# Optimization experiments

Hardware: AMD Instinct MI355X
Metric: run time of the kernel (lower is better)

Reference implementation:

```python
import jax, jax.numpy as jnp
import numpy as np

HIDDEN = 512
HEADS = 8
HEAD_DIM = HIDDEN // HEADS


def setup_inputs() -> dict:
    key = jax.random.key(0)
    ks = jax.random.split(key, 12)
    B, S = 2, 2048
    s = 1.0 / np.sqrt(HIDDEN)
    inp = {
        "query": jax.random.normal(ks[0], (B, S, HIDDEN), dtype=jnp.float32),
        "key": jax.random.normal(ks[1], (B, S, HIDDEN), dtype=jnp.float32),
        "value": jax.random.normal(ks[2], (B, S, HIDDEN), dtype=jnp.float32),
        "Wq": jax.random.uniform(ks[3], (HIDDEN, HIDDEN), jnp.float32, -s, s),
        "bq": jnp.zeros((HIDDEN,), jnp.float32),
        "Wk": jax.random.uniform(ks[4], (HIDDEN, HIDDEN), jnp.float32, -s, s),
        "bk": jnp.zeros((HIDDEN,), jnp.float32),
        "Wv": jax.random.uniform(ks[5], (HIDDEN, HIDDEN), jnp.float32, -s, s),
        "bv": jnp.zeros((HIDDEN,), jnp.float32),
        "Wo": jax.random.uniform(ks[6], (HIDDEN, HIDDEN), jnp.float32, -s, s),
        "bo": jnp.zeros((HIDDEN,), jnp.float32),
    }
    return inp


def reference(query, key, value, Wq, bq, Wk, bk, Wv, bv, Wo, bo):
    B, S, _ = query.shape
    scale = jnp.sqrt(jnp.asarray(HEAD_DIM, dtype=query.dtype))
    # Linear projections (torch Linear: x @ W.T + b)
    Q = (query @ Wq.T + bq).reshape(B, S, HEADS, HEAD_DIM).transpose(0, 2, 1, 3)
    K = (key @ Wk.T + bk).reshape(B, S, HEADS, HEAD_DIM).transpose(0, 2, 1, 3)
    V = (value @ Wv.T + bv).reshape(B, S, HEADS, HEAD_DIM).transpose(0, 2, 1, 3)
    # Scores: [B, H, S, S]
    energy = jnp.einsum("bhqd,bhkd->bhqk", Q, K) / scale
    attn = jax.nn.softmax(energy, axis=-1)
    # Dropout is identity in eval mode.
    x = jnp.einsum("bhqk,bhkd->bhqd", attn, V)
    x = x.transpose(0, 2, 1, 3).reshape(B, S, HIDDEN)
    return x @ Wo.T + bo
```

## Files before the change

kernel.cpp:

```cpp
#include <hip/hip_runtime.h>

typedef __bf16 bf16x8 __attribute__((ext_vector_type(8)));
typedef float f32x4 __attribute__((ext_vector_type(4)));
typedef unsigned int uint4v __attribute__((ext_vector_type(4)));
typedef unsigned int uint2v __attribute__((ext_vector_type(2)));

__device__ __forceinline__ unsigned short f2bf(float f) {
  union { float f; unsigned int u; } v; v.f = f;
  unsigned int u = v.u;
  u += 0x7FFFu + ((u >> 16) & 1u);
  return (unsigned short)(u >> 16);
}

__device__ __forceinline__ unsigned int pack2bf(float a, float b) {
  return (unsigned int)f2bf(a) | ((unsigned int)f2bf(b) << 16);
}

__device__ __forceinline__ unsigned int packtrunc(float a, float b) {
  return __builtin_amdgcn_perm(__float_as_uint(b), __float_as_uint(a),
                               0x07060302u);
}

__global__ __launch_bounds__(256) void convert_w(
    const float* wq, const float* wk, const float* wv, const float* wo,
    unsigned short* wqc, unsigned short* wkc, unsigned short* wvc,
    unsigned short* woc, float qscale)
{
  const float* src; unsigned short* dst; float sc = 1.f;
  switch (blockIdx.y) {
    case 0: src = wq; dst = wqc; sc = qscale; break;
    case 1: src = wk; dst = wkc; break;
    case 2: src = wv; dst = wvc; break;
    default: src = wo; dst = woc; break;
  }
  int idx = (blockIdx.x * 256 + threadIdx.x) * 8;
  f32x4 a = *(const f32x4*)(src + idx);
  f32x4 b = *(const f32x4*)(src + idx + 4);
  uint4v p;
  p.x = pack2bf(a.x * sc, a.y * sc);
  p.y = pack2bf(a.z * sc, a.w * sc);
  p.z = pack2bf(b.x * sc, b.y * sc);
  p.w = pack2bf(b.z * sc, b.w * sc);
  *(uint4v*)(dst + idx) = p;
}

template<int OUT, bool AF32>
__device__ __forceinline__ void gemm_core(
    const void* __restrict__ Ap, const unsigned short* __restrict__ W,
    const float* __restrict__ bias, void* __restrict__ Cp,
    float bscale, int mbase, int nbase)
{
  __shared__ union {
    struct { unsigned short As[2][64][40]; unsigned short Bs[2][128][40]; } t;
    unsigned short Cs[128][72];
  } u;

  const int tid  = threadIdx.x;
  const int wave = tid >> 6, lane = tid & 63;
  const int lrow = lane & 15, lgrp = lane >> 4;
  const int ar = tid >> 2, ac = (tid & 3) * 8;

  const unsigned short* Bg0 = W + (size_t)(nbase + ar) * 512 + ac;
  const unsigned short* Bg1 = W + (size_t)(nbase + ar + 64) * 512 + ac;

  f32x4 acc[4][2];
#pragma unroll
  for (int i = 0; i < 4; i++)
#pragma unroll
    for (int j = 0; j < 2; j++) acc[i][j] = (f32x4){0.f, 0.f, 0.f, 0.f};

  const unsigned short* Ab = (const unsigned short*)Ap;
  const float*          Af = (const float*)Ap;
  uint4v pA; f32x4 pAf0, pAf1;
  if constexpr (AF32) {
    const float* base = Af + (size_t)(mbase + ar) * 512 + ac;
    pAf0 = *(const f32x4*)(base);
    pAf1 = *(const f32x4*)(base + 4);
  } else {
    pA = *(const uint4v*)(Ab + (size_t)(mbase + ar) * 512 + ac);
  }
  uint4v pB0 = *(const uint4v*)Bg0;
  uint4v pB1 = *(const uint4v*)Bg1;

  for (int kt = 0; kt < 512; kt += 32) {
    const int buf = (kt >> 5) & 1;
    if constexpr (AF32) {
      uint4v w;
      w.x = pack2bf(pAf0.x, pAf0.y); w.y = pack2bf(pAf0.z, pAf0.w);
      w.z = pack2bf(pAf1.x, pAf1.y); w.w = pack2bf(pAf1.z, pAf1.w);
      *(uint4v*)&u.t.As[buf][ar][ac] = w;
    } else {
      *(uint4v*)&u.t.As[buf][ar][ac] = pA;
    }
    *(uint4v*)&u.t.Bs[buf][ar][ac]      = pB0;
    *(uint4v*)&u.t.Bs[buf][ar + 64][ac] = pB1;
    if (kt + 32 < 512) {
      if constexpr (AF32) {
        const float* base = Af + (size_t)(mbase + ar) * 512 + ac + kt + 32;
        pAf0 = *(const f32x4*)(base);
        pAf1 = *(const f32x4*)(base + 4);
      } else {
        pA = *(const uint4v*)(Ab + (size_t)(mbase + ar) * 512 + ac + kt + 32);
      }
      pB0 = *(const uint4v*)(Bg0 + kt + 32);
      pB1 = *(const uint4v*)(Bg1 + kt + 32);
    }
    __syncthreads();
    bf16x8 a[4], b[2];
#pragma unroll
    for (int mi = 0; mi < 4; mi++)
      a[mi] = *(const bf16x8*)&u.t.As[buf][mi * 16 + lrow][lgrp * 8];
#pragma unroll
    for (int ni = 0; ni < 2; ni++)
      b[ni] = *(const bf16x8*)&u.t.Bs[buf][wave * 32 + ni * 16 + lrow][lgrp * 8];
#pragma unroll
    for (int mi = 0; mi < 4; mi++)
#pragma unroll
      for (int ni = 0; ni < 2; ni++)
        acc[mi][ni] = __builtin_amdgcn_mfma_f32_16x16x32_bf16(
            a[mi], b[ni], acc[mi][ni], 0, 0, 0);
  }

  if constexpr (OUT == 2) {
    __syncthreads();
#pragma unroll
    for (int ni = 0; ni < 2; ni++) {
      int col_l = wave * 32 + ni * 16 + lrow;
      float bv = bias[nbase + col_l];
#pragma unroll
      for (int mi = 0; mi < 4; mi++) {
        int row_l = mi * 16 + lgrp * 4;
#pragma unroll
        for (int r = 0; r < 4; r++)
          u.Cs[col_l][row_l + r] = f2bf(acc[mi][ni][r] + bv);
      }
    }
    __syncthreads();
    const int bb = mbase >> 11, s_base = mbase & 2047;
    unsigned short* Vt = (unsigned short*)Cp;
#pragma unroll
    for (int ks = 0; ks < 4; ks++) {
      int seg = tid + ks * 256;
      int c = seg >> 3, r0 = (seg & 7) * 8;
      uint4v val = *(const uint4v*)&u.Cs[c][r0];
      int n = nbase + c, hh = n >> 6, d = n & 63;
      *(uint4v*)(Vt + ((size_t)(bb * 8 + hh) * 64 + d) * 2048 + s_base + r0) = val;
    }
  } else {
#pragma unroll
    for (int ni = 0; ni < 2; ni++) {
      int col = nbase + wave * 32 + ni * 16 + lrow;
      float bv = bias[col] * bscale;
#pragma unroll
      for (int mi = 0; mi < 4; mi++) {
        int row0 = mbase + mi * 16 + lgrp * 4;
#pragma unroll
        for (int r = 0; r < 4; r++) {
          float val = acc[mi][ni][r] + bv;
          if constexpr (OUT == 0)
            ((unsigned short*)Cp)[(size_t)(row0 + r) * 512 + col] = f2bf(val);
          else
            ((float*)Cp)[(size_t)(row0 + r) * 512 + col] = val;
        }
      }
    }
  }
}

__global__ __launch_bounds__(256) void qkv_gemm(
    const float* q, const float* k, const float* v,
    const unsigned short* wqc, const unsigned short* wkc,
    const unsigned short* wvc,
    const float* bq, const float* bk, const float* bv,
    unsigned short* Qb, unsigned short* Kb, unsigned short* Vt, float qscale)
{
  const int z = blockIdx.z;
  const int mb = blockIdx.y * 64, nb = blockIdx.x * 128;
  if (z == 2)      gemm_core<2, true>(v, wvc, bv, Vt, 1.f, mb, nb);
  else if (z == 0) gemm_core<0, true>(q, wqc, bq, Qb, qscale, mb, nb);
  else             gemm_core<0, true>(k, wkc, bk, Kb, 1.f, mb, nb);
}

__global__ __launch_bounds__(256) void out_gemm(
    const unsigned short* ctx, const unsigned short* woc,
    const float* bo, float* out)
{
  __shared__ unsigned short As[2][64][40];
  __shared__ unsigned short Bs[2][64][40];

  const int tid  = threadIdx.x;
  const int wave = tid >> 6, lane = tid & 63;
  const int lrow = lane & 15, lgrp = lane >> 4;
  const int mbase = blockIdx.y * 64, nbase = blockIdx.x * 64;
  const int ar = tid >> 2, ac = (tid & 3) * 8;

  const unsigned short* Ag = ctx + (size_t)(mbase + ar) * 512 + ac;
  const unsigned short* Bg = woc + (size_t)(nbase + ar) * 512 + ac;

  f32x4 acc[4];
#pragma unroll
  for (int i = 0; i < 4; i++) acc[i] = (f32x4){0.f, 0.f, 0.f, 0.f};

  uint4v pA = *(const uint4v*)Ag;
  uint4v pB = *(const uint4v*)Bg;

  for (int kt = 0; kt < 512; kt += 32) {
    const int buf = (kt >> 5) & 1;
    *(uint4v*)&As[buf][ar][ac] = pA;
    *(uint4v*)&Bs[buf][ar][ac] = pB;
    if (kt + 32 < 512) {
      pA = *(const uint4v*)(Ag + kt + 32);
      pB = *(const uint4v*)(Bg + kt + 32);
    }
    __syncthreads();
    bf16x8 a[4];
#pragma unroll
    for (int mi = 0; mi < 4; mi++)
      a[mi] = *(const bf16x8*)&As[buf][mi * 16 + lrow][lgrp * 8];
    bf16x8 b = *(const bf16x8*)&Bs[buf][wave * 16 + lrow][lgrp * 8];
#pragma unroll
    for (int mi = 0; mi < 4; mi++)
      acc[mi] = __builtin_amdgcn_mfma_f32_16x16x32_bf16(a[mi], b, acc[mi], 0, 0, 0);
  }

  int col = nbase + wave * 16 + lrow;
  float bv = bo[col];
#pragma unroll
  for (int mi = 0; mi < 4; mi++) {
    int row0 = mbase + mi * 16 + lgrp * 4;
#pragma unroll
    for (int r = 0; r < 4; r++)
      out[(size_t)(row0 + r) * 512 + col] = acc[mi][r] + bv;
  }
}

__global__ __launch_bounds__(256) void attn_kernel(
    const unsigned short* Qb, const unsigned short* Kb,
    const unsigned short* Vt, unsigned short* ctx)
{
  __shared__ unsigned short Ks[2][128][74];
  __shared__ unsigned short Vs[80][138];
  __shared__ unsigned short Ps[2][64][76];

  const int tid  = threadIdx.x;
  const int wave = tid >> 6, lane = tid & 63;
  const int lrow = lane & 15, lgrp = lane >> 4;
  const int qh = wave >> 1, kh = wave & 1;
  const int bh = blockIdx.y, b = bh >> 3, h = bh & 7;
  const int qbase = blockIdx.x * 64;

  const unsigned short* Qg  = Qb + (size_t)(b * 2048 + qbase) * 512 + h * 64;
  const unsigned short* Kg  = Kb + (size_t)(b * 2048) * 512 + h * 64;
  const unsigned short* Vtg = Vt + (size_t)bh * 64 * 2048;

#pragma unroll
  for (int i = 0; i < 2; i++) {
    int seg = tid + i * 256;
    int row = seg >> 3, c0 = (seg & 7) * 8;
    *(uint4v*)&Ps[0][row][c0] = *(const uint4v*)(Qg + (size_t)row * 512 + c0);
  }
  {
    int row = 64 + (tid >> 4), c0 = (tid & 15) * 8;
    unsigned int one2 = 0x3F803F80u;
    *(uint4v*)&Vs[row][c0] = (uint4v){one2, one2, one2, one2};
  }
  __syncthreads();
  bf16x8 qf[2][2];
#pragma unroll
  for (int mi = 0; mi < 2; mi++)
#pragma unroll
    for (int c = 0; c < 2; c++)
      qf[mi][c] = *(const bf16x8*)&Ps[0][qh * 32 + mi * 16 + lrow][c * 32 + lgrp * 8];

  const int s0 = tid >> 3, kc_ = (tid & 7) * 8;
  const int krow0 = ((s0 & 15) << 3) | (s0 >> 4);
  const int vd_ = tid >> 4, vcl = (tid & 15);

  f32x4 oacc[2][5];
#pragma unroll
  for (int mi = 0; mi < 2; mi++)
#pragma unroll
    for (int d = 0; d < 5; d++) oacc[mi][d] = (f32x4){0.f, 0.f, 0.f, 0.f};

  uint4v kr[4], vr[4];
#pragma unroll
  for (int i = 0; i < 4; i++) {
    kr[i] = *(const uint4v*)(Kg + (size_t)(krow0 + 2 * i) * 512 + kc_);
    vr[i] = *(const uint4v*)(Vtg + (size_t)(vd_ + 16 * i) * 2048 + vcl * 8);
  }
#pragma unroll
  for (int i = 0; i < 4; i++) {
    *(uint4v*)&Ks[0][s0 + 32 * i][kc_] = kr[i];
    *(uint2v*)&Vs[vd_ + 16 * i][vcl * 4]      = (uint2v){vr[i].x, vr[i].y};
    *(uint2v*)&Vs[vd_ + 16 * i][64 + vcl * 4] = (uint2v){vr[i].z, vr[i].w};
  }
#pragma unroll
  for (int i = 0; i < 4; i++) {
    kr[i] = *(const uint4v*)(Kg + (size_t)(128 + krow0 + 2 * i) * 512 + kc_);
    vr[i] = *(const uint4v*)(Vtg + (size_t)(vd_ + 16 * i) * 2048 + 128 + vcl * 8);
  }
  __syncthreads();

  for (int it = 0; it < 16; ++it) {
    const int buf = it & 1;
    if (it > 0) {
#pragma unroll
      for (int i = 0; i < 4; i++) {
        *(uint2v*)&Vs[vd_ + 16 * i][vcl * 4]      = (uint2v){vr[i].x, vr[i].y};
        *(uint2v*)&Vs[vd_ + 16 * i][64 + vcl * 4] = (uint2v){vr[i].z, vr[i].w};
      }
      if (it < 15) {
        const int key0 = (it + 1) * 128;
#pragma unroll
        for (int i = 0; i < 4; i++)
          vr[i] = *(const uint4v*)(Vtg + (size_t)(vd_ + 16 * i) * 2048 + key0 + vcl * 8);
      }
    }

    f32x4 sacc[2][4];
#pragma unroll
    for (int mi = 0; mi < 2; mi++)
#pragma unroll
      for (int ni = 0; ni < 4; ni++) sacc[mi][ni] = (f32x4){0.f, 0.f, 0.f, 0.f};
#pragma unroll
    for (int ni = 0; ni < 4; ni++) {
      const int t = 4 * kh + ni;
      bf16x8 k0 = *(const bf16x8*)&Ks[buf][t * 16 + lrow][lgrp * 8];
      bf16x8 k1 = *(const bf16x8*)&Ks[buf][t * 16 + lrow][32 + lgrp * 8];
#pragma unroll
      for (int mi = 0; mi < 2; mi++) {
        sacc[mi][ni] = __builtin_amdgcn_mfma_f32_16x16x32_bf16(qf[mi][0], k0, sacc[mi][ni], 0, 0, 0);
        sacc[mi][ni] = __builtin_amdgcn_mfma_f32_16x16x32_bf16(qf[mi][1], k1, sacc[mi][ni], 0, 0, 0);
      }
    }
#pragma unroll
    for (int mi = 0; mi < 2; mi++)
#pragma unroll
      for (int ni = 0; ni < 4; ni++)
#pragma unroll
        for (int r = 0; r < 4; r++)
          sacc[mi][ni][r] = __builtin_amdgcn_exp2f(sacc[mi][ni][r]);
#pragma unroll
    for (int mi = 0; mi < 2; mi++)
#pragma unroll
      for (int r = 0; r < 4; r++) {
        uint2v pk;
        pk.x = packtrunc(sacc[mi][0][r], sacc[mi][1][r]);
        pk.y = packtrunc(sacc[mi][2][r], sacc[mi][3][r]);
        *(uint2v*)&Ps[kh][qh * 32 + mi * 16 + lgrp * 4 + r][lrow * 4] = pk;
      }

    __syncthreads();

#pragma unroll
    for (int ks = 0; ks < 2; ks++) {
      bf16x8 pa[2];
#pragma unroll
      for (int mi = 0; mi < 2; mi++)
        pa[mi] = *(const bf16x8*)&Ps[kh][qh * 32 + mi * 16 + lrow][ks * 32 + lgrp * 8];
#pragma unroll
      for (int dt = 0; dt < 5; dt++) {
        bf16x8 vb = *(const bf16x8*)&Vs[dt * 16 + lrow][kh * 64 + ks * 32 + lgrp * 8];
#pragma unroll
        for (int mi = 0; mi < 2; mi++)
          oacc[mi][dt] = __builtin_amdgcn_mfma_f32_16x16x32_bf16(pa[mi], vb, oacc[mi][dt], 0, 0, 0);
      }
    }
    if (it < 15) {
#pragma unroll
      for (int i = 0; i < 4; i++)
        *(uint4v*)&Ks[1 - buf][s0 + 32 * i][kc_] = kr[i];
      if (it < 14) {
        const int key0 = (it + 2) * 128;
#pragma unroll
        for (int i = 0; i < 4; i++)
          kr[i] = *(const uint4v*)(Kg + (size_t)(key0 + krow0 + 2 * i) * 512 + kc_);
      }
    }
    __syncthreads();
  }

  float* Obuf = (float*)&Ks[0][0][0];
  float* Lbuf = (float*)&Vs[0][0];
  if (kh == 1) {
#pragma unroll
    for (int mi = 0; mi < 2; mi++)
#pragma unroll
      for (int r = 0; r < 4; r++) {
        int row = qh * 32 + mi * 16 + lgrp * 4 + r;
#pragma unroll
        for (int dt = 0; dt < 4; dt++)
          Obuf[row * 68 + dt * 16 + lrow] = oacc[mi][dt][r];
        if (lrow == 0) Lbuf[row] = oacc[mi][4][r];
      }
  }
  __syncthreads();
  if (kh == 0) {
    unsigned short* Cg = ctx + (size_t)(b * 2048 + qbase) * 512 + h * 64;
#pragma unroll
    for (int mi = 0; mi < 2; mi++)
#pragma unroll
      for (int r = 0; r < 4; r++) {
        int row = qh * 32 + mi * 16 + lgrp * 4 + r;
        float inv = 1.0f / (oacc[mi][4][r] + Lbuf[row]);
#pragma unroll
        for (int dt = 0; dt < 4; dt++) {
          float val = (oacc[mi][dt][r] + Obuf[row * 68 + dt * 16 + lrow]) * inv;
          Cg[(size_t)row * 512 + dt * 16 + lrow] = f2bf(val);
        }
      }
  }
}

extern "C" void kernel_launch(void* const* d_in, const int* in_sizes, int n_in,
                              void* d_out, int out_size, void* d_ws, size_t ws_size,
                              hipStream_t stream)
{
  const float* q  = (const float*)d_in[0];
  const float* k  = (const float*)d_in[1];
  const float* v  = (const float*)d_in[2];
  const float* Wq = (const float*)d_in[3];
  const float* bq = (const float*)d_in[4];
  const float* Wk = (const float*)d_in[5];
  const float* bk = (const float*)d_in[6];
  const float* Wv = (const float*)d_in[7];
  const float* bv = (const float*)d_in[8];
  const float* Wo = (const float*)d_in[9];
  const float* bo = (const float*)d_in[10];
  float* out = (float*)d_out;

  unsigned short* wqc = (unsigned short*)d_ws;
  unsigned short* wkc = wqc + (1 << 18);
  unsigned short* wvc = wkc + (1 << 18);
  unsigned short* woc = wvc + (1 << 18);
  unsigned short* Qb  = woc + (1 << 18);
  unsigned short* Kb  = Qb  + (1 << 21);
  unsigned short* Vt  = Kb  + (1 << 21);
  unsigned short* Cb  = Vt  + (1 << 21);

  const float qscale = 0.125f * 1.44269504088896340736f;

  convert_w<<<dim3(128, 4), 256, 0, stream>>>(
      Wq, Wk, Wv, Wo, wqc, wkc, wvc, woc, qscale);
  qkv_gemm<<<dim3(4, 64, 3), 256, 0, stream>>>(
      q, k, v, wqc, wkc, wvc, bq, bk, bv, Qb, Kb, Vt, qscale);
  attn_kernel<<<dim3(32, 16), 256, 0, stream>>>(Qb, Kb, Vt, Cb);
  out_gemm<<<dim3(8, 64), 256, 0, stream>>>(Cb, woc, bo, out);
}
```

Baseline: 151.4 us.

## Keep attention probabilities in registers via transposed MFMA and permuted V layout

The attention kernel swaps MFMA operand order so the score accumulators come out transposed (keys by queries). This lets the exp'd probabilities be packed straight into B-operand fragments, removing the shared-memory P buffer and one barrier per iteration. The V projection now writes V^T with a permuted sequence order that matches this register layout. K double-buffering is dropped and LDS usage shrinks to allow 3 blocks per CU, the ones-column for the row sums becomes a register constant, and the output is staged through LDS for coalesced stores. In exchange, the global K/V loads get less overlap with compute since there is only a single buffer.

```diff
diff --git a/kernel.cpp b/kernel.cpp
--- a/kernel.cpp
+++ b/kernel.cpp
@@ -19,6 +19,10 @@
 __device__ __forceinline__ unsigned int packtrunc(float a, float b) {
   return __builtin_amdgcn_perm(__float_as_uint(b), __float_as_uint(a),
                                0x07060302u);
+}
+
+__device__ __forceinline__ bf16x8 as_bf(uint4v u) {
+  union { uint4v u; bf16x8 b; } c; c.u = u; return c.b;
 }
 
 __global__ __launch_bounds__(256) void convert_w(
@@ -144,7 +148,11 @@
       int c = seg >> 3, r0 = (seg & 7) * 8;
       uint4v val = *(const uint4v*)&u.Cs[c][r0];
       int n = nbase + c, hh = n >> 6, d = n & 63;
-      *(uint4v*)(Vt + ((size_t)(bb * 8 + hh) * 64 + d) * 2048 + s_base + r0) = val;
+      int sr = s_base + r0;
+      int P0 = (sr & ~31) | (((sr >> 3) & 1) << 4) | (((sr >> 4) & 1) << 2);
+      unsigned short* dst = Vt + ((size_t)(bb * 8 + hh) * 64 + d) * 2048;
+      *(uint2v*)(dst + P0)     = (uint2v){val.x, val.y};
+      *(uint2v*)(dst + P0 + 8) = (uint2v){val.z, val.w};
     }
   } else {
 #pragma unroll
@@ -234,13 +242,12 @@
   }
 }
 
-__global__ __launch_bounds__(256) void attn_kernel(
+__global__ __launch_bounds__(256, 3) void attn_kernel(
     const unsigned short* Qb, const unsigned short* Kb,
     const unsigned short* Vt, unsigned short* ctx)
 {
-  __shared__ unsigned short Ks[2][128][74];
-  __shared__ unsigned short Vs[80][138];
-  __shared__ unsigned short Ps[2][64][76];
+  __shared__ unsigned short Ks[128][74];
+  __shared__ unsigned short Vs[64][134];
 
   const int tid  = threadIdx.x;
   const int wave = tid >> 6, lane = tid & 63;
@@ -257,158 +264,138 @@
   for (int i = 0; i < 2; i++) {
     int seg = tid + i * 256;
     int row = seg >> 3, c0 = (seg & 7) * 8;
-    *(uint4v*)&Ps[0][row][c0] = *(const uint4v*)(Qg + (size_t)row * 512 + c0);
-  }
-  {
-    int row = 64 + (tid >> 4), c0 = (tid & 15) * 8;
-    unsigned int one2 = 0x3F803F80u;
-    *(uint4v*)&Vs[row][c0] = (uint4v){one2, one2, one2, one2};
+    *(uint4v*)&Vs[row][c0] = *(const uint4v*)(Qg + (size_t)row * 512 + c0);
   }
   __syncthreads();
   bf16x8 qf[2][2];
 #pragma unroll
-  for (int mi = 0; mi < 2; mi++)
-#pragma unroll
-    for (int c = 0; c < 2; c++)
-      qf[mi][c] = *(const bf16x8*)&Ps[0][qh * 32 + mi * 16 + lrow][c * 32 + lgrp * 8];
-
-  const int s0 = tid >> 3, kc_ = (tid & 7) * 8;
-  const int krow0 = ((s0 & 15) << 3) | (s0 >> 4);
-  const int vd_ = tid >> 4, vcl = (tid & 15);
+  for (int qt = 0; qt < 2; qt++)
+#pragma unroll
+    for (int ks = 0; ks < 2; ks++)
+      qf[qt][ks] = *(const bf16x8*)&Vs[qh * 32 + qt * 16 + lrow][ks * 32 + lgrp * 8];
+
+  bf16x8 vone;
+  { uint4v o = (uint4v){0x3F803F80u, 0x3F803F80u, 0x3F803F80u, 0x3F803F80u};
+    vone = as_bf(o); }
+
+  const int s0  = tid >> 3, kc_ = (tid & 7) * 8;
+  const int vd0 = tid >> 4, vc_ = (tid & 15) * 8;
 
   f32x4 oacc[2][5];
 #pragma unroll
-  for (int mi = 0; mi < 2; mi++)
-#pragma unroll
-    for (int d = 0; d < 5; d++) oacc[mi][d] = (f32x4){0.f, 0.f, 0.f, 0.f};
+  for (int qt = 0; qt < 2; qt++)
+#pragma unroll
+    for (int d = 0; d < 5; d++) oacc[qt][d] = (f32x4){0.f, 0.f, 0.f, 0.f};
 
   uint4v kr[4], vr[4];
 #pragma unroll
   for (int i = 0; i < 4; i++) {
-    kr[i] = *(const uint4v*)(Kg + (size_t)(krow0 + 2 * i) * 512 + kc_);
-    vr[i] = *(const uint4v*)(Vtg + (size_t)(vd_ + 16 * i) * 2048 + vcl * 8);
-  }
-#pragma unroll
-  for (int i = 0; i < 4; i++) {
-    *(uint4v*)&Ks[0][s0 + 32 * i][kc_] = kr[i];
-    *(uint2v*)&Vs[vd_ + 16 * i][vcl * 4]      = (uint2v){vr[i].x, vr[i].y};
-    *(uint2v*)&Vs[vd_ + 16 * i][64 + vcl * 4] = (uint2v){vr[i].z, vr[i].w};
-  }
-#pragma unroll
-  for (int i = 0; i < 4; i++) {
-    kr[i] = *(const uint4v*)(Kg + (size_t)(128 + krow0 + 2 * i) * 512 + kc_);
-    vr[i] = *(const uint4v*)(Vtg + (size_t)(vd_ + 16 * i) * 2048 + 128 + vcl * 8);
+    kr[i] = *(const uint4v*)(Kg + (size_t)(s0 + 32 * i) * 512 + kc_);
+    vr[i] = *(const uint4v*)(Vtg + (size_t)(vd0 + 16 * i) * 2048 + vc_);
   }
   __syncthreads();
 
   for (int it = 0; it < 16; ++it) {
-    const int buf = it & 1;
-    if (it > 0) {
+#pragma unroll
+    for (int i = 0; i < 4; i++) {
+      *(uint4v*)&Ks[s0 + 32 * i][kc_]  = kr[i];
+      *(uint4v*)&Vs[vd0 + 16 * i][vc_] = vr[i];
+    }
+    __syncthreads();
+    if (it < 15) {
+      const int key0 = (it + 1) * 128;
 #pragma unroll
       for (int i = 0; i < 4; i++) {
-        *(uint2v*)&Vs[vd_ + 16 * i][vcl * 4]      = (uint2v){vr[i].x, vr[i].y};
-        *(uint2v*)&Vs[vd_ + 16 * i][64 + vcl * 4] = (uint2v){vr[i].z, vr[i].w};
-      }
-      if (it < 15) {
-        const int key0 = (it + 1) * 128;
-#pragma unroll
-        for (int i = 0; i < 4; i++)
-          vr[i] = *(const uint4v*)(Vtg + (size_t)(vd_ + 16 * i) * 2048 + key0 + vcl * 8);
+        kr[i] = *(const uint4v*)(Kg + (size_t)(key0 + s0 + 32 * i) * 512 + kc_);
+        vr[i] = *(const uint4v*)(Vtg + (size_t)(vd0 + 16 * i) * 2048 + key0 + vc_);
       }
     }
 
     f32x4 sacc[2][4];
 #pragma unroll
-    for (int mi = 0; mi < 2; mi++)
-#pragma unroll
-      for (int ni = 0; ni < 4; ni++) sacc[mi][ni] = (f32x4){0.f, 0.f, 0.f, 0.f};
-#pragma unroll
-    for (int ni = 0; ni < 4; ni++) {
-      const int t = 4 * kh + ni;
-      bf16x8 k0 = *(const bf16x8*)&Ks[buf][t * 16 + lrow][lgrp * 8];
-      bf16x8 k1 = *(const bf16x8*)&Ks[buf][t * 16 + lrow][32 + lgrp * 8];
-#pragma unroll
-      for (int mi = 0; mi < 2; mi++) {
-        sacc[mi][ni] = __builtin_amdgcn_mfma_f32_16x16x32_bf16(qf[mi][0], k0, sacc[mi][ni], 0, 0, 0);
-        sacc[mi][ni] = __builtin_amdgcn_mfma_f32_16x16x32_bf16(qf[mi][1], k1, sacc[mi][ni], 0, 0, 0);
-      }
-    }
-#pragma unroll
-    for (int mi = 0; mi < 2; mi++)
-#pragma unroll
-      for (int ni = 0; ni < 4; ni++)
+    for (int qt = 0; qt < 2; qt++)
+#pragma unroll
+      for (int kt = 0; kt < 4; kt++) sacc[qt][kt] = (f32x4){0.f, 0.f, 0.f, 0.f};
+#pragma unroll
+    for (int kt = 0; kt < 4; kt++) {
+      bf16x8 a0 = *(const bf16x8*)&Ks[kh * 64 + kt * 16 + lrow][lgrp * 8];
+      bf16x8 a1 = *(const bf16x8*)&Ks[kh * 64 + kt * 16 + lrow][32 + lgrp * 8];
+#pragma unroll
+      for (int qt = 0; qt < 2; qt++) {
+        sacc[qt][kt] = __builtin_amdgcn_mfma_f32_16x16x32_bf16(a0, qf[qt][0], sacc[qt][kt], 0, 0, 0);
+        sacc[qt][kt] = __builtin_amdgcn_mfma_f32_16x16x32_bf16(a1, qf[qt][1], sacc[qt][kt], 0, 0, 0);
+      }
+    }
+
+#pragma unroll
+    for (int qt = 0; qt < 2; qt++)
+#pragma unroll
+      for (int kt = 0; kt < 4; kt++)
 #pragma unroll
         for (int r = 0; r < 4; r++)
-          sacc[mi][ni][r] = __builtin_amdgcn_exp2f(sacc[mi][ni][r]);
-#pragma unroll
-    for (int mi = 0; mi < 2; mi++)
-#pragma unroll
-      for (int r = 0; r < 4; r++) {
-        uint2v pk;
-        pk.x = packtrunc(sacc[mi][0][r], sacc[mi][1][r]);
-        pk.y = packtrunc(sacc[mi][2][r], sacc[mi][3][r]);
-        *(uint2v*)&Ps[kh][qh * 32 + mi * 16 + lgrp * 4 + r][lrow * 4] = pk;
-      }
-
-    __syncthreads();
-
-#pragma unroll
-    for (int ks = 0; ks < 2; ks++) {
-      bf16x8 pa[2];
-#pragma unroll
-      for (int mi = 0; mi < 2; mi++)
-        pa[mi] = *(const bf16x8*)&Ps[kh][qh * 32 + mi * 16 + lrow][ks * 32 + lgrp * 8];
+          sacc[qt][kt][r] = __builtin_amdgcn_exp2f(sacc[qt][kt][r]);
+
+#pragma unroll
+    for (int c = 0; c < 2; c++) {
+      bf16x8 pf[2];
+#pragma unroll
+      for (int qt = 0; qt < 2; qt++) {
+        uint4v pk;
+        pk.x = packtrunc(sacc[qt][2 * c][0],     sacc[qt][2 * c][1]);
+        pk.y = packtrunc(sacc[qt][2 * c][2],     sacc[qt][2 * c][3]);
+        pk.z = packtrunc(sacc[qt][2 * c + 1][0], sacc[qt][2 * c + 1][1]);
+        pk.w = packtrunc(sacc[qt][2 * c + 1][2], sacc[qt][2 * c + 1][3]);
+        pf[qt] = as_bf(pk);
+      }
 #pragma unroll
       for (int dt = 0; dt < 5; dt++) {
-        bf16x8 vb = *(const bf16x8*)&Vs[dt * 16 + lrow][kh * 64 + ks * 32 + lgrp * 8];
-#pragma unroll
-        for (int mi = 0; mi < 2; mi++)
-          oacc[mi][dt] = __builtin_amdgcn_mfma_f32_16x16x32_bf16(pa[mi], vb, oacc[mi][dt], 0, 0, 0);
-      }
-    }
-    if (it < 15) {
-#pragma unroll
-      for (int i = 0; i < 4; i++)
-        *(uint4v*)&Ks[1 - buf][s0 + 32 * i][kc_] = kr[i];
-      if (it < 14) {
-        const int key0 = (it + 2) * 128;
-#pragma unroll
-        for (int i = 0; i < 4; i++)
-          kr[i] = *(const uint4v*)(Kg + (size_t)(key0 + krow0 + 2 * i) * 512 + kc_);
-      }
-    }
-    __syncthreads();
-  }
-
-  float* Obuf = (float*)&Ks[0][0][0];
-  float* Lbuf = (float*)&Vs[0][0];
+        bf16x8 vb = (dt < 4)
+          ? *(const bf16x8*)&Vs[dt * 16 + lrow][(2 * kh + c) * 32 + lgrp * 8]
+          : vone;
+#pragma unroll
+        for (int qt = 0; qt < 2; qt++)
+          oacc[qt][dt] = __builtin_amdgcn_mfma_f32_16x16x32_bf16(vb, pf[qt], oacc[qt][dt], 0, 0, 0);
+      }
+    }
+    __syncthreads();
+  }
+
+  float* Obuf = (float*)&Ks[0][0];
+  float* Lbuf = Obuf + 64 * 68;
   if (kh == 1) {
 #pragma unroll
-    for (int mi = 0; mi < 2; mi++)
-#pragma unroll
-      for (int r = 0; r < 4; r++) {
-        int row = qh * 32 + mi * 16 + lgrp * 4 + r;
-#pragma unroll
-        for (int dt = 0; dt < 4; dt++)
-          Obuf[row * 68 + dt * 16 + lrow] = oacc[mi][dt][r];
-        if (lrow == 0) Lbuf[row] = oacc[mi][4][r];
-      }
+    for (int qt = 0; qt < 2; qt++) {
+      int qrow = qh * 32 + qt * 16 + lrow;
+#pragma unroll
+      for (int dt = 0; dt < 4; dt++)
+#pragma unroll
+        for (int r = 0; r < 4; r++)
+          Obuf[qrow * 68 + dt * 16 + lgrp * 4 + r] = oacc[qt][dt][r];
+      if (lgrp == 0) Lbuf[qrow] = oacc[qt][4][0];
+    }
   }
   __syncthreads();
   if (kh == 0) {
-    unsigned short* Cg = ctx + (size_t)(b * 2048 + qbase) * 512 + h * 64;
-#pragma unroll
-    for (int mi = 0; mi < 2; mi++)
-#pragma unroll
-      for (int r = 0; r < 4; r++) {
-        int row = qh * 32 + mi * 16 + lgrp * 4 + r;
-        float inv = 1.0f / (oacc[mi][4][r] + Lbuf[row]);
-#pragma unroll
-        for (int dt = 0; dt < 4; dt++) {
-          float val = (oacc[mi][dt][r] + Obuf[row * 68 + dt * 16 + lrow]) * inv;
-          Cg[(size_t)row * 512 + dt * 16 + lrow] = f2bf(val);
+#pragma unroll
+    for (int qt = 0; qt < 2; qt++) {
+      int qrow = qh * 32 + qt * 16 + lrow;
+      float inv = 1.0f / (oacc[qt][4][0] + Lbuf[qrow]);
+#pragma unroll
+      for (int dt = 0; dt < 4; dt++)
+#pragma unroll
+        for (int r = 0; r < 4; r++) {
+          float val = (oacc[qt][dt][r] + Obuf[qrow * 68 + dt * 16 + lgrp * 4 + r]) * inv;
+          Vs[qrow][dt * 16 + lgrp * 4 + r] = f2bf(val);
         }
-      }
+    }
+  }
+  __syncthreads();
+  unsigned short* Cg = ctx + (size_t)(b * 2048 + qbase) * 512 + h * 64;
+#pragma unroll
+  for (int i = 0; i < 2; i++) {
+    int seg = tid + i * 256;
+    int row = seg >> 3, c0 = (seg & 7) * 8;
+    *(uint4v*)(Cg + (size_t)row * 512 + c0) = *(const uint4v*)&Vs[row][c0];
   }
 }
 
```

Result: faster. 144.9 us (-4.3%).
